# Performance work log

Measured on AMD Instinct MI355X. Metric: run time of the kernel, lower is better.

The kernel has to match this reference:

```python
import jax, jax.numpy as jnp
import numpy as np


def _lstm_scan(x_tbd, Wih, Whh, bih, bhh):
    """Standard LSTM cell (PyTorch i,f,g,o gate order) scanned over time.
    x_tbd: [T,B,D]; returns hidden states [T,B,H]."""
    H = Whh.shape[1]
    B = x_tbd.shape[1]

    def step(carry, x_t):
        h, c = carry
        gates = x_t @ Wih.T + bih + h @ Whh.T + bhh  # [B,4H]
        i, f, g, o = jnp.split(gates, 4, axis=-1)
        c = jax.nn.sigmoid(f) * c + jax.nn.sigmoid(i) * jnp.tanh(g)
        h = jax.nn.sigmoid(o) * jnp.tanh(c)
        return (h, c), h

    h0 = jnp.zeros((B, H), x_tbd.dtype)
    _, hs = jax.lax.scan(step, (h0, h0), x_tbd)
    return hs


def setup_inputs() -> dict:
    key = jax.random.key(0)
    B, T, D, H = 64, 1024, 512, 256  # output_dim=1024 -> H = output_dim//4 per direction
    ks = jax.random.split(key, 9)
    s = 0.05
    mk = lambda k, shape: jax.random.normal(k, shape, jnp.float32) * s
    return {
        "input": mk(ks[0], (B, T, D)),
        "Wih_f": mk(ks[1], (4 * H, D)), "Whh_f": mk(ks[2], (4 * H, H)),
        "bih_f": mk(ks[3], (4 * H,)),   "bhh_f": mk(ks[4], (4 * H,)),
        "Wih_b": mk(ks[5], (4 * H, D)), "Whh_b": mk(ks[6], (4 * H, H)),
        "bih_b": mk(ks[7], (4 * H,)),   "bhh_b": mk(ks[8], (4 * H,)),
    }


def reference(input, Wih_f, Whh_f, bih_f, bhh_f, Wih_b, Whh_b, bih_b, bhh_b):
    # [B,T,D] -> [T,B,D] for scan over time
    x_tbd = jnp.transpose(input, (1, 0, 2))
    hf = _lstm_scan(x_tbd, Wih_f, Whh_f, bih_f, bhh_f)            # forward in time
    hb = _lstm_scan(x_tbd[::-1], Wih_b, Whh_b, bih_b, bhh_b)[::-1]  # backward, re-aligned
    # output[t] = cat(outputf[t], outputb[T-1-t]) == cat(hf[t], hb_aligned[t])
    out = jnp.concatenate([hf, hb], axis=-1)  # [T,B,2H]
    return jnp.transpose(out, (1, 0, 2))      # [B,T,2H]
```

## Files before the change

kernel.cpp:

```cpp
#include <hip/hip_runtime.h>
#include <hip/hip_bf16.h>

typedef __attribute__((ext_vector_type(8))) short bf8;
typedef __attribute__((ext_vector_type(4))) float f32x4;
typedef __attribute__((ext_vector_type(4))) unsigned int u32x4;

#define T_SEQ 1024

__device__ __forceinline__ float sigm(float x) { return 1.f / (1.f + __expf(-x)); }
__device__ __forceinline__ float tanh_(float x) { return 2.f / (1.f + __expf(-2.f * x)) - 1.f; }

__device__ __forceinline__ short bf16s(float x) {
    union { __hip_bfloat16 h; short s; } u;
    u.h = __float2bfloat16(x);
    return u.s;
}

__device__ __forceinline__ bf8 pack_bf8(const float4 a, const float4 b) {
    bf8 r;
    r[0] = bf16s(a.x); r[1] = bf16s(a.y); r[2] = bf16s(a.z); r[3] = bf16s(a.w);
    r[4] = bf16s(b.x); r[5] = bf16s(b.y); r[6] = bf16s(b.z); r[7] = bf16s(b.w);
    return r;
}

__device__ __forceinline__ void store_sc1_b32(void* p, unsigned int v) {
    asm volatile("global_store_dword %0, %1, off sc1" :: "v"(p), "v"(v) : "memory");
}
__device__ __forceinline__ unsigned int load_sc1_b32(const void* p) {
    unsigned int v;
    asm volatile("global_load_dword %0, %1, off sc1\n"
                 "s_waitcnt vmcnt(0)"
                 : "=v"(v) : "v"(p) : "memory");
    return v;
}
__device__ __forceinline__ u32x4 load_sc1_x4(const void* p) {
    u32x4 v;
    asm volatile("global_load_dwordx4 %0, %1, off sc1" : "=v"(v) : "v"(p) : "memory");
    return v;
}

__device__ __forceinline__ unsigned short ldnt_u16(const __hip_bfloat16* p) {
    return __builtin_nontemporal_load((const unsigned short*)p);
}

__global__ __launch_bounds__(256) void init_kernel(unsigned int* __restrict__ p, int n)
{
    const int i = blockIdx.x * 256 + threadIdx.x;
    if (i < n) p[i] = 0u;
}

__global__ __launch_bounds__(256) void xproj_kernel(
    const float* __restrict__ X,
    const float* __restrict__ WihF,
    const float* __restrict__ bihF,
    const float* __restrict__ bhhF,
    const float* __restrict__ WihB,
    const float* __restrict__ bihB,
    const float* __restrict__ bhhB,
    __hip_bfloat16* __restrict__ XpF,
    __hip_bfloat16* __restrict__ XpB)
{
    const int dir = blockIdx.z;
    const float* W  = dir ? WihB : WihF;
    const float* bi = dir ? bihB : bihF;
    const float* bh = dir ? bhhB : bhhF;
    __hip_bfloat16* Xp = dir ? XpB : XpF;

    __shared__ __align__(16) short As[128 * 32];
    __shared__ __align__(16) short Bs[128 * 32];

    const int tid  = threadIdx.x;
    const int lane = tid & 63;
    const int w    = tid >> 6;
    const int quad = lane >> 4;
    const int l16  = lane & 15;
    const int wr   = w >> 1, wc = w & 1;

    const int m0 = blockIdx.x * 128;
    const int n0 = blockIdx.y * 128;

    const int srow = tid >> 2;
    const int scg  = tid & 3;

    f32x4 acc[4][4] = {};

    for (int kk = 0; kk < 512; kk += 32) {
        const float* pa0 = X + (size_t)(m0 + srow)      * 512 + kk + scg * 8;
        const float* pa1 = X + (size_t)(m0 + 64 + srow) * 512 + kk + scg * 8;
        const float* pb0 = W + (size_t)(n0 + srow)      * 512 + kk + scg * 8;
        const float* pb1 = W + (size_t)(n0 + 64 + srow) * 512 + kk + scg * 8;
        bf8 a0 = pack_bf8(*(const float4*)pa0, *(const float4*)(pa0 + 4));
        bf8 a1 = pack_bf8(*(const float4*)pa1, *(const float4*)(pa1 + 4));
        bf8 b0 = pack_bf8(*(const float4*)pb0, *(const float4*)(pb0 + 4));
        bf8 b1 = pack_bf8(*(const float4*)pb1, *(const float4*)(pb1 + 4));
        __syncthreads();
        *(bf8*)&As[(srow)      * 32 + scg * 8] = a0;
        *(bf8*)&As[(64 + srow) * 32 + scg * 8] = a1;
        *(bf8*)&Bs[(srow)      * 32 + scg * 8] = b0;
        *(bf8*)&Bs[(64 + srow) * 32 + scg * 8] = b1;
        __syncthreads();

        bf8 af[4], bfr[4];
#pragma unroll
        for (int mt = 0; mt < 4; mt++)
            af[mt] = *(const bf8*)&As[(wr * 64 + mt * 16 + l16) * 32 + quad * 8];
#pragma unroll
        for (int nt = 0; nt < 4; nt++)
            bfr[nt] = *(const bf8*)&Bs[(wc * 64 + nt * 16 + l16) * 32 + quad * 8];
#pragma unroll
        for (int mt = 0; mt < 4; mt++)
#pragma unroll
            for (int nt = 0; nt < 4; nt++)
                acc[mt][nt] = __builtin_amdgcn_mfma_f32_16x16x32_bf16(af[mt], bfr[nt], acc[mt][nt], 0, 0, 0);
    }

#pragma unroll
    for (int nt = 0; nt < 4; nt++) {
        const int n = n0 + wc * 64 + nt * 16 + l16;
        const float bias = bi[n] + bh[n];
        const int g = n >> 8, s = (n >> 4) & 15, j = n & 15;
#pragma unroll
        for (int mt = 0; mt < 4; mt++) {
#pragma unroll
            for (int r = 0; r < 4; r++) {
                const int m = m0 + wr * 64 + mt * 16 + quad * 4 + r;
                const int b = m >> 10, t = m & 1023;
                Xp[((((size_t)t * 16 + s) * 64 + b) * 4 + g) * 16 + j] =
                    __float2bfloat16(acc[mt][nt][r] + bias);
            }
        }
    }
}

__global__ __launch_bounds__(256, 1) void lstm_rec_kernel(
    const __hip_bfloat16* __restrict__ XpF,
    const __hip_bfloat16* __restrict__ XpB,
    const float* __restrict__ WhhF,
    const float* __restrict__ WhhB,
    unsigned int* __restrict__ ex,
    float* __restrict__ out)
{
    const int wg  = blockIdx.x;
    const int dir = wg >> 4;
    const int s   = wg & 15;
    const int tid  = threadIdx.x;
    const int lane = tid & 63;
    const int w    = tid >> 6;
    const int quad = lane >> 4;
    const int l16  = lane & 15;

    const __hip_bfloat16* Xp = dir ? XpB : XpF;
    const float* Whh         = dir ? WhhB : WhhF;

    bf8 Bf[4][8];
#pragma unroll
    for (int g = 0; g < 4; g++)
#pragma unroll
        for (int k = 0; k < 8; k++) {
            const float* p = Whh + (size_t)(g * 256 + s * 16 + l16) * 256 + k * 32 + quad * 8;
            Bf[g][k] = pack_bf8(*(const float4*)p, *(const float4*)(p + 4));
        }

    float c[4] = {0.f, 0.f, 0.f, 0.f};

    const int crow = quad >> 1;
    const int coff = (w * 16 + l16) * 16 + (quad & 1) * 8;
    unsigned int* const exdir = ex + (dir << 14);

    for (int tau = 0; tau < T_SEQ; tau++) {
        const int t = dir ? (T_SEQ - 1 - tau) : tau;

        const __hip_bfloat16* xrow = Xp + ((((size_t)t * 16 + s) * 64 + w * 16) * 4) * 16;
        unsigned short xpu[4][4];
#pragma unroll
        for (int g = 0; g < 4; g++)
#pragma unroll
            for (int r = 0; r < 4; r++)
                xpu[g][r] = ldnt_u16(&xrow[((quad * 4 + r) * 4 + g) * 16 + l16]);

        const unsigned int tagv = (unsigned int)tau;
        const unsigned int tagw = tagv << 16;
        unsigned int* const exc = exdir + ((tau & 1) << 15);

        {
            const unsigned int* probep = exc + (lane & 15) * 1024 + w * 256 + 255;
            int guard = 0;
            while (true) {
                const unsigned int pv = load_sc1_b32(probep);
                if (__all((int)((pv >> 16) == tagv))) break;
                if (++guard >= 4096) break;
            }
        }

        u32x4 dd[16];
        int bguard = 0;
        while (true) {
#pragma unroll
            for (int k8 = 0; k8 < 8; k8++) {
                dd[2 * k8]     = load_sc1_x4(exc + (k8 * 2 + crow) * 1024 + coff);
                dd[2 * k8 + 1] = load_sc1_x4(exc + (k8 * 2 + crow) * 1024 + coff + 4);
            }
            asm volatile("s_waitcnt vmcnt(0)" ::: "memory");
            __builtin_amdgcn_sched_barrier(0);
            unsigned int diff = 0;
#pragma unroll
            for (int i = 0; i < 16; i++) {
                diff |= (dd[i][0] ^ tagw) & 0xFFFF0000u;
                diff |= (dd[i][1] ^ tagw) & 0xFFFF0000u;
                diff |= (dd[i][2] ^ tagw) & 0xFFFF0000u;
                diff |= (dd[i][3] ^ tagw) & 0xFFFF0000u;
            }
            if (__all((int)(diff == 0u))) break;
            if (++bguard >= 256) break;
        }

        bf8 Af[8];
#pragma unroll
        for (int k8 = 0; k8 < 8; k8++) {
#pragma unroll
            for (int j = 0; j < 4; j++) {
                Af[k8][j]     = (short)(dd[2 * k8][j]     & 0xFFFFu);
                Af[k8][4 + j] = (short)(dd[2 * k8 + 1][j] & 0xFFFFu);
            }
        }

        f32x4 acc[4];
        const f32x4 zero = {0.f, 0.f, 0.f, 0.f};
#pragma unroll
        for (int g = 0; g < 4; g++) acc[g] = zero;
#pragma unroll
        for (int k = 0; k < 8; k++)
#pragma unroll
            for (int g = 0; g < 4; g++)
                acc[g] = __builtin_amdgcn_mfma_f32_16x16x32_bf16(Af[k], Bf[g][k], acc[g], 0, 0, 0);

        const unsigned int pubtag = (unsigned int)(tau + 1) << 16;
        unsigned int* const dst = exdir + (((tau + 1) & 1) << 15) + (s << 10);
        float hv[4];
#pragma unroll
        for (int r = 0; r < 4; r++) {
            union { unsigned int u; float f; } cv0, cv1, cv2, cv3;
            cv0.u = (unsigned int)xpu[0][r] << 16;
            cv1.u = (unsigned int)xpu[1][r] << 16;
            cv2.u = (unsigned int)xpu[2][r] << 16;
            cv3.u = (unsigned int)xpu[3][r] << 16;
            const float ig = sigm(acc[0][r] + cv0.f);
            const float fg = sigm(acc[1][r] + cv1.f);
            const float gg = tanh_(acc[2][r] + cv2.f);
            const float og = sigm(acc[3][r] + cv3.f);
            c[r] = fg * c[r] + ig * gg;
            hv[r] = og * tanh_(c[r]);
            const int b = w * 16 + quad * 4 + r;
            store_sc1_b32(&dst[b * 16 + l16],
                          pubtag | (unsigned int)(unsigned short)bf16s(hv[r]));
        }

#pragma unroll
        for (int r = 0; r < 4; r++) {
            const int b = w * 16 + quad * 4 + r;
            __builtin_nontemporal_store(hv[r], &out[((size_t)b * T_SEQ + t) * 512 + dir * 256 + s * 16 + l16]);
        }
    }
}

extern "C" void kernel_launch(void* const* d_in, const int* in_sizes, int n_in,
                              void* d_out, int out_size, void* d_ws, size_t ws_size,
                              hipStream_t stream)
{
    const float* X    = (const float*)d_in[0];
    const float* WihF = (const float*)d_in[1];
    const float* WhhF = (const float*)d_in[2];
    const float* bihF = (const float*)d_in[3];
    const float* bhhF = (const float*)d_in[4];
    const float* WihB = (const float*)d_in[5];
    const float* WhhB = (const float*)d_in[6];
    const float* bihB = (const float*)d_in[7];
    const float* bhhB = (const float*)d_in[8];
    float* out = (float*)d_out;

    char* ws = (char*)d_ws;
    __hip_bfloat16* XpF = (__hip_bfloat16*)ws;
    __hip_bfloat16* XpB = (__hip_bfloat16*)(ws + 134217728);
    unsigned int*   ex  = (unsigned int*)(ws + 268435456);

    const int initN = 65536;
    init_kernel<<<initN / 256, 256, 0, stream>>>(ex, initN);

    dim3 g1(512, 8, 2);
    xproj_kernel<<<g1, 256, 0, stream>>>(X, WihF, bihF, bhhF, WihB, bihB, bhhB, XpF, XpB);
    lstm_rec_kernel<<<32, 256, 0, stream>>>(XpF, XpB, WhhF, WhhB, ex, out);
}
```

Baseline: 4.919 ms.

## Interleave forward and backward LSTM directions within each recurrent workgroup

Each workgroup now handles one hidden slice for both directions, so 16 workgroups launch instead of 32, and each holds both directions' Whh fragments in registers. Inside each timestep it processes the forward and then the backward direction. While one direction waits for peers to publish, the other direction's work can proceed, and a grid-wide exchange involves fewer workgroups. The handshake is also reordered: it loads the tagged data optimistically first and only falls back to probe-and-retry loops if the tags do not match. In exchange, each workgroup does double the work per step, the doubled Bf array raises register pressure with risk of spills, and the two directions are serialised within a step.

```diff
diff --git a/kernel.cpp b/kernel.cpp
--- a/kernel.cpp
+++ b/kernel.cpp
@@ -140,61 +140,52 @@
     unsigned int* __restrict__ ex,
     float* __restrict__ out)
 {
-    const int wg  = blockIdx.x;
-    const int dir = wg >> 4;
-    const int s   = wg & 15;
+    const int s    = blockIdx.x;
     const int tid  = threadIdx.x;
     const int lane = tid & 63;
     const int w    = tid >> 6;
     const int quad = lane >> 4;
     const int l16  = lane & 15;
 
-    const __hip_bfloat16* Xp = dir ? XpB : XpF;
-    const float* Whh         = dir ? WhhB : WhhF;
-
-    bf8 Bf[4][8];
-#pragma unroll
-    for (int g = 0; g < 4; g++)
-#pragma unroll
-        for (int k = 0; k < 8; k++) {
-            const float* p = Whh + (size_t)(g * 256 + s * 16 + l16) * 256 + k * 32 + quad * 8;
-            Bf[g][k] = pack_bf8(*(const float4*)p, *(const float4*)(p + 4));
-        }
-
-    float c[4] = {0.f, 0.f, 0.f, 0.f};
+    bf8 Bf[2][4][8];
+#pragma unroll
+    for (int dir = 0; dir < 2; dir++) {
+        const float* Whh = dir ? WhhB : WhhF;
+#pragma unroll
+        for (int g = 0; g < 4; g++)
+#pragma unroll
+            for (int k = 0; k < 8; k++) {
+                const float* p = Whh + (size_t)(g * 256 + s * 16 + l16) * 256 + k * 32 + quad * 8;
+                Bf[dir][g][k] = pack_bf8(*(const float4*)p, *(const float4*)(p + 4));
+            }
+    }
+
+    float c[2][4] = {};
 
     const int crow = quad >> 1;
     const int coff = (w * 16 + l16) * 16 + (quad & 1) * 8;
-    unsigned int* const exdir = ex + (dir << 14);
 
     for (int tau = 0; tau < T_SEQ; tau++) {
-        const int t = dir ? (T_SEQ - 1 - tau) : tau;
-
-        const __hip_bfloat16* xrow = Xp + ((((size_t)t * 16 + s) * 64 + w * 16) * 4) * 16;
-        unsigned short xpu[4][4];
-#pragma unroll
-        for (int g = 0; g < 4; g++)
-#pragma unroll
-            for (int r = 0; r < 4; r++)
-                xpu[g][r] = ldnt_u16(&xrow[((quad * 4 + r) * 4 + g) * 16 + l16]);
-
         const unsigned int tagv = (unsigned int)tau;
         const unsigned int tagw = tagv << 16;
-        unsigned int* const exc = exdir + ((tau & 1) << 15);
-
-        {
-            const unsigned int* probep = exc + (lane & 15) * 1024 + w * 256 + 255;
-            int guard = 0;
-            while (true) {
-                const unsigned int pv = load_sc1_b32(probep);
-                if (__all((int)((pv >> 16) == tagv))) break;
-                if (++guard >= 4096) break;
-            }
-        }
-
-        u32x4 dd[16];
-        int bguard = 0;
-        while (true) {
+        const unsigned int pubtag = (unsigned int)(tau + 1) << 16;
+
+#pragma unroll
+        for (int dir = 0; dir < 2; dir++) {
+            const int t = dir ? (T_SEQ - 1 - tau) : tau;
+            const __hip_bfloat16* Xp = dir ? XpB : XpF;
+            unsigned int* const exdir = ex + (dir << 14);
+            unsigned int* const exc   = exdir + ((tau & 1) << 15);
+
+            const __hip_bfloat16* xrow = Xp + ((((size_t)t * 16 + s) * 64 + w * 16) * 4) * 16;
+            unsigned short xpu[4][4];
+#pragma unroll
+            for (int g = 0; g < 4; g++)
+#pragma unroll
+                for (int r = 0; r < 4; r++)
+                    xpu[g][r] = ldnt_u16(&xrow[((quad * 4 + r) * 4 + g) * 16 + l16]);
+
+            u32x4 dd[16];
 #pragma unroll
             for (int k8 = 0; k8 < 8; k8++) {
                 dd[2 * k8]     = load_sc1_x4(exc + (k8 * 2 + crow) * 1024 + coff);
@@ -210,55 +201,72 @@
                 diff |= (dd[i][2] ^ tagw) & 0xFFFF0000u;
                 diff |= (dd[i][3] ^ tagw) & 0xFFFF0000u;
             }
-            if (__all((int)(diff == 0u))) break;
-            if (++bguard >= 256) break;
-        }
-
-        bf8 Af[8];
-#pragma unroll
-        for (int k8 = 0; k8 < 8; k8++) {
-#pragma unroll
-            for (int j = 0; j < 4; j++) {
-                Af[k8][j]     = (short)(dd[2 * k8][j]     & 0xFFFFu);
-                Af[k8][4 + j] = (short)(dd[2 * k8 + 1][j] & 0xFFFFu);
-            }
-        }
-
-        f32x4 acc[4];
-        const f32x4 zero = {0.f, 0.f, 0.f, 0.f};
-#pragma unroll
-        for (int g = 0; g < 4; g++) acc[g] = zero;
-#pragma unroll
-        for (int k = 0; k < 8; k++)
-#pragma unroll
-            for (int g = 0; g < 4; g++)
-                acc[g] = __builtin_amdgcn_mfma_f32_16x16x32_bf16(Af[k], Bf[g][k], acc[g], 0, 0, 0);
-
-        const unsigned int pubtag = (unsigned int)(tau + 1) << 16;
-        unsigned int* const dst = exdir + (((tau + 1) & 1) << 15) + (s << 10);
-        float hv[4];
-#pragma unroll
-        for (int r = 0; r < 4; r++) {
-            union { unsigned int u; float f; } cv0, cv1, cv2, cv3;
-            cv0.u = (unsigned int)xpu[0][r] << 16;
-            cv1.u = (unsigned int)xpu[1][r] << 16;
-            cv2.u = (unsigned int)xpu[2][r] << 16;
-            cv3.u = (unsigned int)xpu[3][r] << 16;
-            const float ig = sigm(acc[0][r] + cv0.f);
-            const float fg = sigm(acc[1][r] + cv1.f);
-            const float gg = tanh_(acc[2][r] + cv2.f);
-            const float og = sigm(acc[3][r] + cv3.f);
-            c[r] = fg * c[r] + ig * gg;
-            hv[r] = og * tanh_(c[r]);
-            const int b = w * 16 + quad * 4 + r;
-            store_sc1_b32(&dst[b * 16 + l16],
-                          pubtag | (unsigned int)(unsigned short)bf16s(hv[r]));
-        }
-
-#pragma unroll
-        for (int r = 0; r < 4; r++) {
-            const int b = w * 16 + quad * 4 + r;
-            __builtin_nontemporal_store(hv[r], &out[((size_t)b * T_SEQ + t) * 512 + dir * 256 + s * 16 + l16]);
+            bool ok = __all((int)(diff == 0u));
+
+            int outer = 0;
+            while (!ok && ++outer < 64) {
+                const unsigned int* probep = exc + (lane & 15) * 1024 + w * 256 + 255;
+                int guard = 0;
+                while (true) {
+                    const unsigned int pv = load_sc1_b32(probep);
+                    if (__all((int)((pv >> 16) == tagv))) break;
+                    if (++guard >= 8192) break;
+                }
+#pragma unroll
+                for (int k8 = 0; k8 < 8; k8++) {
+                    dd[2 * k8]     = load_sc1_x4(exc + (k8 * 2 + crow) * 1024 + coff);
+                    dd[2 * k8 + 1] = load_sc1_x4(exc + (k8 * 2 + crow) * 1024 + coff + 4);
+                }
+                asm volatile("s_waitcnt vmcnt(0)" ::: "memory");
+                __builtin_amdgcn_sched_barrier(0);
+                diff = 0;
+#pragma unroll
+                for (int i = 0; i < 16; i++) {
+                    diff |= (dd[i][0] ^ tagw) & 0xFFFF0000u;
+                    diff |= (dd[i][1] ^ tagw) & 0xFFFF0000u;
+                    diff |= (dd[i][2] ^ tagw) & 0xFFFF0000u;
+                    diff |= (dd[i][3] ^ tagw) & 0xFFFF0000u;
+                }
+                ok = __all((int)(diff == 0u));
+            }
+
+            f32x4 acc[4];
+            const f32x4 zero = {0.f, 0.f, 0.f, 0.f};
+#pragma unroll
+            for (int g = 0; g < 4; g++) acc[g] = zero;
+#pragma unroll
+            for (int k8 = 0; k8 < 8; k8++) {
+                bf8 Af;
+#pragma unroll
+                for (int j = 0; j < 4; j++) {
+                    Af[j]     = (short)(dd[2 * k8][j]     & 0xFFFFu);
+                    Af[4 + j] = (short)(dd[2 * k8 + 1][j] & 0xFFFFu);
+                }
+#pragma unroll
+                for (int g = 0; g < 4; g++)
+                    acc[g] = __builtin_amdgcn_mfma_f32_16x16x32_bf16(Af, Bf[dir][g][k8], acc[g], 0, 0, 0);
+            }
+
+            unsigned int* const dst = exdir + (((tau + 1) & 1) << 15) + (s << 10);
+#pragma unroll
+            for (int r = 0; r < 4; r++) {
+                union { unsigned int u; float f; } cv0, cv1, cv2, cv3;
+                cv0.u = (unsigned int)xpu[0][r] << 16;
+                cv1.u = (unsigned int)xpu[1][r] << 16;
+                cv2.u = (unsigned int)xpu[2][r] << 16;
+                cv3.u = (unsigned int)xpu[3][r] << 16;
+                const float ig = sigm(acc[0][r] + cv0.f);
+                const float fg = sigm(acc[1][r] + cv1.f);
+                const float gg = tanh_(acc[2][r] + cv2.f);
+                const float og = sigm(acc[3][r] + cv3.f);
+                c[dir][r] = fg * c[dir][r] + ig * gg;
+                const float hv = og * tanh_(c[dir][r]);
+                const int b = w * 16 + quad * 4 + r;
+                store_sc1_b32(&dst[b * 16 + l16],
+                              pubtag | (unsigned int)(unsigned short)bf16s(hv));
+                __builtin_nontemporal_store(
+                    hv, &out[((size_t)b * T_SEQ + t) * 512 + dir * 256 + s * 16 + l16]);
+            }
         }
     }
 }
@@ -288,5 +296,5 @@
 
     dim3 g1(512, 8, 2);
     xproj_kernel<<<g1, 256, 0, stream>>>(X, WihF, bihF, bhhF, WihB, bihB, bhhB, XpF, XpB);
-    lstm_rec_kernel<<<32, 256, 0, stream>>>(XpF, XpB, WhhF, WhhB, ex, out);
-}
+    lstm_rec_kernel<<<16, 256, 0, stream>>>(XpF, XpB, WhhF, WhhB, ex, out);
+}
```

New measurement: 7.671 ms. +55.9%, slower.
